# Performance work log

Hardware: AMD Instinct MI355X
Metric: run time of the kernel (lower is better)

## Reference

```python
import jax, jax.numpy as jnp
import numpy as np

N = 50000      # num_nodes
E = 400000     # num_edges
H = 64         # h_dim
R = 200        # num_rels
B = 8          # num_bases (block-diagonal decomposition)


def setup_inputs() -> dict:
    ks = jax.random.split(jax.random.key(0), 10)
    s = 1.0 / np.sqrt(H).astype(np.float32)
    return {
        "emb":     jax.random.normal(ks[0], (N, H), jnp.float32),
        "norm":    jax.random.uniform(ks[1], (E, 1), jnp.float32),
        "eps":     jax.random.normal(ks[2], (N, H), jnp.float32),
        "w1":      jax.random.normal(ks[3], (R, B * 8 * 8), jnp.float32) * s,
        "loop_w1": jax.random.normal(ks[4], (H, H), jnp.float32) * s,
        "b1":      jnp.zeros((H,), jnp.float32),
        "w2":      jax.random.normal(ks[5], (R, B * 8 * 16), jnp.float32) * s,
        "loop_w2": jax.random.normal(ks[6], (H, 2 * H), jnp.float32) * s,
        "b2":      jnp.zeros((2 * H,), jnp.float32),
        "h_ids":   jnp.arange(N, dtype=jnp.int32),
        "src":     jax.random.randint(ks[7], (E,), 0, N, jnp.int32),
        "dst":     jax.random.randint(ks[8], (E,), 0, N, jnp.int32),
        "rel":     jax.random.randint(ks[9], (E,), 0, R, jnp.int32),
    }


def bdd_conv(feat, src, dst, rel, norm, weight, loop_w, bias, out_feat):
    # RelGraphConv with 'bdd' regularizer: per-edge relation-indexed
    # block-diagonal weight gather, bmm message, norm scale, scatter-add,
    # then bias + self-loop.
    n_edges = src.shape[0]
    sub_in = feat.shape[1] // B
    sub_out = out_feat // B
    w = weight[rel].reshape(n_edges, B, sub_in, sub_out)   # gather per edge
    x = feat[src].reshape(n_edges, B, sub_in)
    msg = jnp.einsum('ebi,ebio->ebo', x, w).reshape(n_edges, out_feat) * norm
    agg = jax.ops.segment_sum(msg, dst, num_segments=feat.shape[0])
    return agg + bias + feat @ loop_w


def reference(emb, norm, eps, w1, loop_w1, b1, w2, loop_w2, b2,
              h_ids, src, dst, rel):
    feat = emb[h_ids]                                       # embedding lookup
    h1 = jax.nn.relu(bdd_conv(feat, src, dst, rel, norm, w1, loop_w1, b1, H))
    h2 = bdd_conv(h1, src, dst, rel, norm, w2, loop_w2, b2, 2 * H)
    m, raw_v = jnp.split(h2, 2, axis=-1)                    # gaussian_parameters
    v = jax.nn.softplus(raw_v) + 1e-8
    return m + jnp.sqrt(v) * eps                            # reparameterize
```

## Files before the change

kernel.cpp:

```cpp
#include <hip/hip_runtime.h>
#include <math.h>


typedef __attribute__((ext_vector_type(8))) short bf16x8;
typedef __attribute__((ext_vector_type(4))) float f32x4;
typedef __attribute__((ext_vector_type(2))) _Float16 h2;

__device__ __forceinline__ int bcasti(int v, int l) { return __builtin_amdgcn_readlane(v, l); }
__device__ __forceinline__ float bcastf(float v, int l) {
    return __int_as_float(__builtin_amdgcn_readlane(__float_as_int(v), l));
}
__device__ __forceinline__ unsigned short f2bf(float f) {
    unsigned u = __float_as_uint(f);
    return (unsigned short)((u + 0x7FFFu + ((u >> 16) & 1u)) >> 16);
}
__device__ __forceinline__ unsigned short f2h16(float f) {
    return __builtin_bit_cast(unsigned short, (_Float16)f);
}
__device__ __forceinline__ float bfs(unsigned short s) { return __uint_as_float((unsigned)s << 16); }
__device__ __forceinline__ h2 uh2(unsigned u) { return __builtin_bit_cast(h2, u); }


__global__ __launch_bounds__(256) void
blockhist(const int* __restrict__ dst, const int* __restrict__ rel,
          int* __restrict__ deg, int* __restrict__ bh, int R, int NB2, int e) {
    __shared__ int h[256];
    int t = threadIdx.x, b = blockIdx.x;
    h[t] = 0;
    __syncthreads();
    int base = b * 1024;
#pragma unroll
    for (int k = 0; k < 4; ++k) {
        int i = base + k * 256 + t;
        if (i < e) {
            atomicAdd(&deg[dst[i]], 1);
            atomicAdd(&h[rel[i]], 1);
        }
    }
    __syncthreads();
    if (t < R) bh[(size_t)t * NB2 + b] = h[t];
}

__global__ __launch_bounds__(256) void
rel_scan(int* __restrict__ bh, int* __restrict__ degr, int NB2) {
    __shared__ int sm[256];
    int r = blockIdx.x, t = threadIdx.x;
    int carry = 0;
    for (int s = 0; s < NB2; s += 256) {
        int idx = s + t;
        int v = (idx < NB2) ? bh[(size_t)r * NB2 + idx] : 0;
        sm[t] = v;
        __syncthreads();
        for (int d = 1; d < 256; d <<= 1) {
            int u = (t >= d) ? sm[t - d] : 0;
            __syncthreads();
            sm[t] += u;
            __syncthreads();
        }
        if (idx < NB2) bh[(size_t)r * NB2 + idx] = carry + sm[t] - v;
        int tot = sm[255];
        __syncthreads();
        carry += tot;
    }
    if (t == 0) degr[r] = carry;
}

__global__ void scan_part(const int* __restrict__ deg, int* __restrict__ bsum, int n) {
    __shared__ int sm[256];
    int t = threadIdx.x, g = blockIdx.x * 256 + t;
    sm[t] = (g < n) ? deg[g] : 0;
    __syncthreads();
    for (int d = 128; d > 0; d >>= 1) {
        if (t < d) sm[t] += sm[t + d];
        __syncthreads();
    }
    if (t == 0) bsum[blockIdx.x] = sm[0];
}

__global__ void scan_bsum(int* __restrict__ bsum, int* __restrict__ off, int nb, int n) {
    __shared__ int sm[256];
    int t = threadIdx.x;
    int v = (t < nb) ? bsum[t] : 0;
    sm[t] = v;
    __syncthreads();
    for (int d = 1; d < 256; d <<= 1) {
        int u = (t >= d) ? sm[t - d] : 0;
        __syncthreads();
        sm[t] += u;
        __syncthreads();
    }
    if (t < nb) bsum[t] = sm[t] - v;
    if (t == 255) off[n] = sm[255];
}

__global__ void scan_write(const int* __restrict__ deg, const int* __restrict__ bsum,
                           int* __restrict__ off, int n) {
    __shared__ int sm[256];
    int t = threadIdx.x, g = blockIdx.x * 256 + t;
    int v = (g < n) ? deg[g] : 0;
    sm[t] = v;
    __syncthreads();
    for (int d = 1; d < 256; d <<= 1) {
        int u = (t >= d) ? sm[t - d] : 0;
        __syncthreads();
        sm[t] += u;
        __syncthreads();
    }
    if (g < n) off[g] = bsum[blockIdx.x] + sm[t] - v;
}

__global__ void scan_rel(const int* __restrict__ degr, int* __restrict__ offr, int R) {
    __shared__ int sm[256];
    int t = threadIdx.x;
    int v = (t < R) ? degr[t] : 0;
    sm[t] = v;
    __syncthreads();
    for (int d = 1; d < 256; d <<= 1) {
        int u = (t >= d) ? sm[t - d] : 0;
        __syncthreads();
        sm[t] += u;
        __syncthreads();
    }
    if (t < R) offr[t] = sm[t] - v;
    if (t == 255) offr[R] = sm[255];
}

__global__ __launch_bounds__(256) void
scatter3(const int* __restrict__ src, const int* __restrict__ dst,
         const int* __restrict__ rel, const float* __restrict__ norm,
         const int* __restrict__ h_ids, const int* __restrict__ off,
         const int* __restrict__ offr, const int* __restrict__ bh,
         int* __restrict__ fil, int* __restrict__ pos,
         int* __restrict__ xidA, int* __restrict__ xidB,
         float* __restrict__ nrm, int NB2, int e) {
    __shared__ int h[256];
    int t = threadIdx.x, b = blockIdx.x;
    h[t] = 0;
    __syncthreads();
    int base = b * 1024;
#pragma unroll
    for (int k = 0; k < 4; ++k) {
        int i = base + k * 256 + t;
        if (i < e) {
            int r = rel[i], d = dst[i], s = src[i];
            int lr = atomicAdd(&h[r], 1);
            int p = offr[r] + bh[(size_t)r * NB2 + b] + lr;
            int q = off[d] + atomicAdd(&fil[d], 1);
            pos[q] = p;
            xidA[p] = h_ids[s];
            xidB[p] = s;
            nrm[p] = norm[i];
        }
    }
}


__global__ void cvt_new(const float* __restrict__ w1, const float* __restrict__ w2,
                        const float* __restrict__ emb, unsigned short* __restrict__ w1dT,
                        unsigned short* __restrict__ w2dT, unsigned short* __restrict__ embh,
                        int R, int ne) {
    int i = blockIdx.x * blockDim.x + threadIdx.x;
    int n1d = R * 4096, n2d = R * 8192;
    if (i < n1d) {
        int r = i >> 12, rem = i & 4095;
        int c = rem >> 6, k = rem & 63;
        int b = k >> 3;
        float v = (b == (c >> 3)) ? w1[(size_t)r * 512 + b * 64 + (k & 7) * 8 + (c & 7)] : 0.f;
        w1dT[i] = f2bf(v);
    } else if (i < n1d + n2d) {
        int ii = i - n1d;
        int r = ii >> 13, rem = ii & 8191;
        int c = rem >> 6, k = rem & 63;
        int b = k >> 3;
        float v = (b == (c >> 4)) ? w2[(size_t)r * 1024 + b * 128 + (k & 7) * 16 + (c & 15)] : 0.f;
        w2dT[ii] = f2bf(v);
    } else if (i < n1d + n2d + ne) {
        int ii = i - n1d - n2d;
        embh[ii] = f2bf(emb[ii]);
    }
}

__global__ void cvt_old(const float* __restrict__ w1, const float* __restrict__ w2,
                        const float* __restrict__ emb, unsigned short* __restrict__ w1h,
                        unsigned short* __restrict__ w2h, unsigned short* __restrict__ embh,
                        int n1, int n2, int ne) {
    int i = blockIdx.x * blockDim.x + threadIdx.x;
    if (i < n1) w1h[i] = f2h16(w1[i]);
    else if (i < n1 + n2) w2h[i - n1] = f2h16(w2[i - n1]);
    else if (i < n1 + n2 + ne) embh[i - n1 - n2] = f2bf(emb[i - n1 - n2]);
}


__global__ __launch_bounds__(256) void
gemm1_mfma(const unsigned short* __restrict__ embh, const int* __restrict__ h_ids,
           const float* __restrict__ lw1, const float* __restrict__ b1,
           unsigned short* __restrict__ h1bh, int n_nodes) {
    int w = threadIdx.x >> 6, l = threadIdx.x & 63;
    int lr = l & 15, lq = l >> 4;
    int rt = blockIdx.x;
    bf16x8 bfr[2];
    int coln = w * 16 + lr;
#pragma unroll
    for (int kb = 0; kb < 2; ++kb)
#pragma unroll
        for (int jj = 0; jj < 8; ++jj)
            bfr[kb][jj] = (short)f2bf(lw1[(kb * 32 + lq * 8 + jj) * 64 + coln]);
    int nrow = rt * 16 + lr;
    if (nrow >= n_nodes) nrow = n_nodes - 1;
    const unsigned short* arow = embh + (long)h_ids[nrow] * 64 + lq * 8;
    bf16x8 af0 = *(const bf16x8*)arow;
    bf16x8 af1 = *(const bf16x8*)(arow + 32);
    f32x4 acc = {0.f, 0.f, 0.f, 0.f};
    acc = __builtin_amdgcn_mfma_f32_16x16x32_bf16(af0, bfr[0], acc, 0, 0, 0);
    acc = __builtin_amdgcn_mfma_f32_16x16x32_bf16(af1, bfr[1], acc, 0, 0, 0);
    float bb = b1[coln];
#pragma unroll
    for (int r = 0; r < 4; ++r) {
        int row = rt * 16 + lq * 4 + r;
        if (row < n_nodes) h1bh[(long)row * 64 + coln] = f2bf(acc[r] + bb);
    }
}

__global__ __launch_bounds__(256) void
gemm2_mfma(const unsigned short* __restrict__ h1h, const float* __restrict__ lw2,
           const float* __restrict__ b2, unsigned short* __restrict__ h2bh, int n_nodes) {
    int w = threadIdx.x >> 6, l = threadIdx.x & 63;
    int lr = l & 15, lq = l >> 4;
    int rt = blockIdx.x;
    bf16x8 bfr[2][2];
    int col0 = (2 * w) * 16 + lr, col1 = (2 * w + 1) * 16 + lr;
#pragma unroll
    for (int kb = 0; kb < 2; ++kb)
#pragma unroll
        for (int jj = 0; jj < 8; ++jj) {
            int k = kb * 32 + lq * 8 + jj;
            bfr[0][kb][jj] = (short)f2bf(lw2[k * 128 + col0]);
            bfr[1][kb][jj] = (short)f2bf(lw2[k * 128 + col1]);
        }
    int nrow = rt * 16 + lr;
    if (nrow >= n_nodes) nrow = n_nodes - 1;
    bf16x8 af0 = *(const bf16x8*)(h1h + (long)nrow * 64 + lq * 8);
    bf16x8 af1 = *(const bf16x8*)(h1h + (long)nrow * 64 + 32 + lq * 8);
    f32x4 acc0 = {0.f, 0.f, 0.f, 0.f}, acc1 = {0.f, 0.f, 0.f, 0.f};
    acc0 = __builtin_amdgcn_mfma_f32_16x16x32_bf16(af0, bfr[0][0], acc0, 0, 0, 0);
    acc0 = __builtin_amdgcn_mfma_f32_16x16x32_bf16(af1, bfr[0][1], acc0, 0, 0, 0);
    acc1 = __builtin_amdgcn_mfma_f32_16x16x32_bf16(af0, bfr[1][0], acc1, 0, 0, 0);
    acc1 = __builtin_amdgcn_mfma_f32_16x16x32_bf16(af1, bfr[1][1], acc1, 0, 0, 0);
    float bb0 = b2[col0], bb1 = b2[col1];
#pragma unroll
    for (int r = 0; r < 4; ++r) {
        int row = rt * 16 + lq * 4 + r;
        if (row < n_nodes) {
            h2bh[(long)row * 128 + col0] = f2bf(acc0[r] + bb0);
            h2bh[(long)row * 128 + col1] = f2bf(acc1[r] + bb1);
        }
    }
}


__global__ __launch_bounds__(256) void
gemm_rel1(const unsigned short* __restrict__ embh, const unsigned short* __restrict__ w1dT,
          const int* __restrict__ xidA, const float* __restrict__ nrm,
          const int* __restrict__ offr, _Float16* __restrict__ msg1, int S) {
    int r = blockIdx.x / S, s = blockIdx.x % S;
    int w = threadIdx.x >> 6, l = threadIdx.x & 63;
    int lr = l & 15, lq = l >> 4;
    int e0r = offr[r], e1r = offr[r + 1];
    if (e0r >= e1r) return;
    bf16x8 bfr[4][2];
    const unsigned short* wb = w1dT + (size_t)r * 4096;
#pragma unroll
    for (int ct = 0; ct < 4; ++ct)
#pragma unroll
        for (int kb = 0; kb < 2; ++kb)
            bfr[ct][kb] = *(const bf16x8*)(wb + (ct * 16 + lr) * 64 + kb * 32 + lq * 8);
    for (int t = s * 4 + w;; t += S * 4) {
        int t16 = e0r + t * 16;
        if (t16 >= e1r) break;
        int erow = t16 + lr;
        int erc = erow < e1r ? erow : e1r - 1;
        const unsigned short* arow = embh + (size_t)xidA[erc] * 64 + lq * 8;
        bf16x8 af0 = *(const bf16x8*)arow;
        bf16x8 af1 = *(const bf16x8*)(arow + 32);
        f32x4 acc[4];
#pragma unroll
        for (int ct = 0; ct < 4; ++ct) {
            acc[ct] = (f32x4){0.f, 0.f, 0.f, 0.f};
            acc[ct] = __builtin_amdgcn_mfma_f32_16x16x32_bf16(af0, bfr[ct][0], acc[ct], 0, 0, 0);
            acc[ct] = __builtin_amdgcn_mfma_f32_16x16x32_bf16(af1, bfr[ct][1], acc[ct], 0, 0, 0);
        }
#pragma unroll
        for (int r4 = 0; r4 < 4; ++r4) {
            int orow = t16 + lq * 4 + r4;
            int orc = orow < e1r ? orow : e1r - 1;
            float nm = nrm[orc];
            if (orow < e1r) {
#pragma unroll
                for (int ct = 0; ct < 4; ++ct)
                    msg1[(size_t)orow * 64 + ct * 16 + lr] = (_Float16)(acc[ct][r4] * nm);
            }
        }
    }
}

__global__ __launch_bounds__(256) void
gemm_rel2(const unsigned short* __restrict__ h1h, const unsigned short* __restrict__ w2dT,
          const int* __restrict__ xidB, const float* __restrict__ nrm,
          const int* __restrict__ offr, _Float16* __restrict__ msg2, int S) {
    int r = blockIdx.x / S, s = blockIdx.x % S;
    int w = threadIdx.x >> 6, l = threadIdx.x & 63;
    int lr = l & 15, lq = l >> 4;
    int e0r = offr[r], e1r = offr[r + 1];
    if (e0r >= e1r) return;
    bf16x8 bfr[8][2];
    const unsigned short* wb = w2dT + (size_t)r * 8192;
#pragma unroll
    for (int ct = 0; ct < 8; ++ct)
#pragma unroll
        for (int kb = 0; kb < 2; ++kb)
            bfr[ct][kb] = *(const bf16x8*)(wb + (ct * 16 + lr) * 64 + kb * 32 + lq * 8);
    for (int t = s * 4 + w;; t += S * 4) {
        int t16 = e0r + t * 16;
        if (t16 >= e1r) break;
        int erow = t16 + lr;
        int erc = erow < e1r ? erow : e1r - 1;
        const unsigned short* arow = h1h + (size_t)xidB[erc] * 64 + lq * 8;
        bf16x8 af0 = *(const bf16x8*)arow;
        bf16x8 af1 = *(const bf16x8*)(arow + 32);
        f32x4 acc[8];
#pragma unroll
        for (int ct = 0; ct < 8; ++ct) {
            acc[ct] = (f32x4){0.f, 0.f, 0.f, 0.f};
            acc[ct] = __builtin_amdgcn_mfma_f32_16x16x32_bf16(af0, bfr[ct][0], acc[ct], 0, 0, 0);
            acc[ct] = __builtin_amdgcn_mfma_f32_16x16x32_bf16(af1, bfr[ct][1], acc[ct], 0, 0, 0);
        }
#pragma unroll
        for (int r4 = 0; r4 < 4; ++r4) {
            int orow = t16 + lq * 4 + r4;
            int orc = orow < e1r ? orow : e1r - 1;
            float nm = nrm[orc];
            if (orow < e1r) {
#pragma unroll
                for (int ct = 0; ct < 8; ++ct)
                    msg2[(size_t)orow * 128 + ct * 16 + lr] = (_Float16)(acc[ct][r4] * nm);
            }
        }
    }
}


__global__ __launch_bounds__(256) void
sum1(const _Float16* __restrict__ msg1, const int* __restrict__ pos,
     const unsigned short* __restrict__ h1bh, const int* __restrict__ off,
     unsigned short* __restrict__ h1h, int n_nodes) {
    int tid = threadIdx.x;
    int w = tid >> 6, j = tid & 63;
    int n = blockIdx.x * 4 + w;
    if (n >= n_nodes) return;
    float base = bfs(h1bh[(size_t)n * 64 + j]);
    int e0 = off[n], e1v = off[n + 1];
    float a0 = 0.f, a1 = 0.f, a2 = 0.f, a3 = 0.f;
    for (int win = e0; win < e1v; win += 64) {
        int wcnt = e1v - win; if (wcnt > 64) wcnt = 64;
        int pv = (j < wcnt) ? pos[win + j] : 0;
        int c = 0;
        for (; c + 4 <= wcnt; c += 4) {
            int p0 = bcasti(pv, c), p1 = bcasti(pv, c + 1);
            int p2 = bcasti(pv, c + 2), p3 = bcasti(pv, c + 3);
            a0 += (float)msg1[(size_t)p0 * 64 + j];
            a1 += (float)msg1[(size_t)p1 * 64 + j];
            a2 += (float)msg1[(size_t)p2 * 64 + j];
            a3 += (float)msg1[(size_t)p3 * 64 + j];
        }
        for (; c < wcnt; ++c)
            a0 += (float)msg1[(size_t)bcasti(pv, c) * 64 + j];
    }
    float s = a0 + a1 + a2 + a3 + base;
    h1h[(size_t)n * 64 + j] = f2bf(fmaxf(s, 0.f));
}

__global__ __launch_bounds__(256) void
sum2(const _Float16* __restrict__ msg2, const int* __restrict__ pos,
     const unsigned short* __restrict__ h2bh, const float* __restrict__ eps,
     const int* __restrict__ off, float* __restrict__ out, int n_nodes) {
    int tid = threadIdx.x;
    int w = tid >> 6, j = tid & 63;
    int n = blockIdx.x * 4 + w;
    if (n >= n_nodes) return;
    float basem = bfs(h2bh[(size_t)n * 128 + j]);
    float basev = bfs(h2bh[(size_t)n * 128 + 64 + j]);
    int e0 = off[n], e1v = off[n + 1];
    float m0 = 0.f, m1 = 0.f, v0 = 0.f, v1a = 0.f;
    for (int win = e0; win < e1v; win += 64) {
        int wcnt = e1v - win; if (wcnt > 64) wcnt = 64;
        int pv = (j < wcnt) ? pos[win + j] : 0;
        int c = 0;
        for (; c + 2 <= wcnt; c += 2) {
            int p0 = bcasti(pv, c), p1 = bcasti(pv, c + 1);
            m0 += (float)msg2[(size_t)p0 * 128 + j];
            v0 += (float)msg2[(size_t)p0 * 128 + 64 + j];
            m1 += (float)msg2[(size_t)p1 * 128 + j];
            v1a += (float)msg2[(size_t)p1 * 128 + 64 + j];
        }
        for (; c < wcnt; ++c) {
            int p0 = bcasti(pv, c);
            m0 += (float)msg2[(size_t)p0 * 128 + j];
            v0 += (float)msg2[(size_t)p0 * 128 + 64 + j];
        }
    }
    float vm = m0 + m1 + basem;
    float vv = v0 + v1a + basev;
    float sp = (vv > 20.f) ? vv : log1pf(expf(vv));
    out[(size_t)n * 64 + j] = fmaf(sqrtf(sp + 1e-8f), eps[(size_t)n * 64 + j], vm);
}


__global__ void hist2(const int* __restrict__ dst, const int* __restrict__ rel,
                      int* __restrict__ deg, int* __restrict__ degr, int e) {
    int i = blockIdx.x * blockDim.x + threadIdx.x;
    if (i < e) {
        atomicAdd(&deg[dst[i]], 1);
        atomicAdd(&degr[rel[i]], 1);
    }
}

__global__ void scatter_pack(const int* __restrict__ src, const int* __restrict__ dst,
                             const int* __restrict__ rel, const float* __restrict__ norm,
                             const int* __restrict__ h_ids, const int* __restrict__ off,
                             int* __restrict__ fil, unsigned* __restrict__ packA,
                             unsigned* __restrict__ packB, float* __restrict__ norm_s, int e) {
    int i = blockIdx.x * blockDim.x + threadIdx.x;
    if (i >= e) return;
    int d = dst[i];
    int p = off[d] + atomicAdd(&fil[d], 1);
    unsigned rhi = (unsigned)rel[i] << 16;
    int s = src[i];
    packA[p] = (unsigned)h_ids[s] | rhi;
    packB[p] = (unsigned)s | rhi;
    norm_s[p] = norm[i];
}

__device__ __forceinline__ float reduce8(float a0, float a1, float a2, float a3,
                                         float a4, float a5, float a6, float a7, int i) {
    int p1 = i & 1, p2 = (i >> 1) & 1, p3 = (i >> 2) & 1;
    float ka, sb, u0, u1, u2, u3, w0, w1;
    ka = p1 ? a1 : a0; sb = p1 ? a0 : a1; u0 = ka + __shfl_xor(sb, 1, 64);
    ka = p1 ? a3 : a2; sb = p1 ? a2 : a3; u1 = ka + __shfl_xor(sb, 1, 64);
    ka = p1 ? a5 : a4; sb = p1 ? a4 : a5; u2 = ka + __shfl_xor(sb, 1, 64);
    ka = p1 ? a7 : a6; sb = p1 ? a6 : a7; u3 = ka + __shfl_xor(sb, 1, 64);
    ka = p2 ? u1 : u0; sb = p2 ? u0 : u1; w0 = ka + __shfl_xor(sb, 2, 64);
    ka = p2 ? u3 : u2; sb = p2 ? u2 : u3; w1 = ka + __shfl_xor(sb, 2, 64);
    ka = p3 ? w1 : w0; sb = p3 ? w0 : w1;
    return ka + __shfl_xor(sb, 4, 64);
}

__global__ __launch_bounds__(256) void
edge1(const unsigned short* __restrict__ embh, const unsigned short* __restrict__ w1h,
      const unsigned short* __restrict__ h1bh, const int* __restrict__ off,
      const unsigned* __restrict__ packA, const float* __restrict__ norm_s,
      unsigned short* __restrict__ h1h, int n_nodes) {
    __shared__ unsigned short xstage[4][8][64];
    int tid = threadIdx.x;
    int w = tid >> 6, j = tid & 63, i = j & 7;
    int cl = j >> 3, il = j & 7;
    int n = blockIdx.x * 4 + w;
    if (n >= n_nodes) return;
    unsigned short* xsw = &xstage[w][0][0];
    float base = bfs(h1bh[(long)n * 64 + j]);
    h2 acc[4];
#pragma unroll
    for (int q = 0; q < 4; ++q) acc[q] = (h2){(_Float16)0.f, (_Float16)0.f};
    int e0 = off[n], e1v = off[n + 1];
    const long woff = (long)j * 8;
    for (int win = e0; win < e1v; win += 64) {
        int wcnt = e1v - win; if (wcnt > 64) wcnt = 64;
        unsigned u = (j < wcnt) ? packA[win + j] : 0u;
        float nmv = (j < wcnt) ? norm_s[win + j] : 0.f;
        for (int b8 = 0; b8 < wcnt; b8 += 8) {
            int cnt = wcnt - b8; if (cnt > 8) cnt = 8;
            int uc = __builtin_amdgcn_ds_bpermute((b8 + cl) << 2, (int)u);
            if (cl < cnt)
                *(bf16x8*)(xsw + (cl << 6) + (il << 3)) =
                    *(const bf16x8*)(embh + (long)((unsigned)uc & 0xFFFFu) * 64 + (il << 3));
            asm volatile("s_waitcnt lgkmcnt(0)" ::: "memory");
#pragma unroll
            for (int c = 0; c < 8; ++c)
                if (c < cnt) {
                    float nm = bcastf(nmv, b8 + c);
                    int rr = bcasti((int)u, b8 + c) >> 16;
                    uint4 wd = *(const uint4*)(w1h + (long)rr * 512 + woff);
                    _Float16 xh = (_Float16)(bfs(xsw[(c << 6) + j]) * nm);
                    h2 xh2 = {xh, xh};
                    acc[0] += xh2 * uh2(wd.x);
                    acc[1] += xh2 * uh2(wd.y);
                    acc[2] += xh2 * uh2(wd.z);
                    acc[3] += xh2 * uh2(wd.w);
                }
        }
    }
    float agg = reduce8((float)acc[0].x, (float)acc[0].y, (float)acc[1].x, (float)acc[1].y,
                        (float)acc[2].x, (float)acc[2].y, (float)acc[3].x, (float)acc[3].y, i);
    h1h[(long)n * 64 + j] = f2bf(fmaxf(base + agg, 0.f));
}

__global__ __launch_bounds__(256) void
edge2(const unsigned short* __restrict__ h1h, const unsigned short* __restrict__ w2h,
      const unsigned short* __restrict__ h2bh, const float* __restrict__ eps,
      const int* __restrict__ off, const unsigned* __restrict__ packB,
      const float* __restrict__ norm_s, float* __restrict__ out, int n_nodes) {
    __shared__ unsigned short xstage[4][8][64];
    int tid = threadIdx.x;
    int w = tid >> 6, j = tid & 63;
    int i = j & 7, b = j >> 3;
    int o1 = b * 16 + i, o2 = o1 + 8;
    int cl = j >> 3, il = j & 7;
    int n = blockIdx.x * 4 + w;
    if (n >= n_nodes) return;
    unsigned short* xsw = &xstage[w][0][0];
    float base1 = bfs(h2bh[(long)n * 128 + o1]);
    float base2 = bfs(h2bh[(long)n * 128 + o2]);
    h2 acc[8];
#pragma unroll
    for (int q = 0; q < 8; ++q) acc[q] = (h2){(_Float16)0.f, (_Float16)0.f};
    int e0 = off[n], e1v = off[n + 1];
    const long woff = (long)j * 16;
    for (int win = e0; win < e1v; win += 64) {
        int wcnt = e1v - win; if (wcnt > 64) wcnt = 64;
        unsigned u = (j < wcnt) ? packB[win + j] : 0u;
        float nmv = (j < wcnt) ? norm_s[win + j] : 0.f;
        for (int b8 = 0; b8 < wcnt; b8 += 8) {
            int cnt = wcnt - b8; if (cnt > 8) cnt = 8;
            int uc = __builtin_amdgcn_ds_bpermute((b8 + cl) << 2, (int)u);
            if (cl < cnt)
                *(bf16x8*)(xsw + (cl << 6) + (il << 3)) =
                    *(const bf16x8*)(h1h + (long)((unsigned)uc & 0xFFFFu) * 64 + (il << 3));
            asm volatile("s_waitcnt lgkmcnt(0)" ::: "memory");
#pragma unroll
            for (int c = 0; c < 8; ++c)
                if (c < cnt) {
                    float nm = bcastf(nmv, b8 + c);
                    int rr = bcasti((int)u, b8 + c) >> 16;
                    const uint4* p = (const uint4*)(w2h + (long)rr * 1024 + woff);
                    uint4 wa = p[0], wb = p[1];
                    _Float16 xh = (_Float16)(bfs(xsw[(c << 6) + j]) * nm);
                    h2 xh2 = {xh, xh};
                    acc[0] += xh2 * uh2(wa.x);
                    acc[1] += xh2 * uh2(wa.y);
                    acc[2] += xh2 * uh2(wa.z);
                    acc[3] += xh2 * uh2(wa.w);
                    acc[4] += xh2 * uh2(wb.x);
                    acc[5] += xh2 * uh2(wb.y);
                    acc[6] += xh2 * uh2(wb.z);
                    acc[7] += xh2 * uh2(wb.w);
                }
        }
    }
    float r1 = reduce8((float)acc[0].x, (float)acc[0].y, (float)acc[1].x, (float)acc[1].y,
                       (float)acc[2].x, (float)acc[2].y, (float)acc[3].x, (float)acc[3].y, i);
    float r2 = reduce8((float)acc[4].x, (float)acc[4].y, (float)acc[5].x, (float)acc[5].y,
                       (float)acc[6].x, (float)acc[6].y, (float)acc[7].x, (float)acc[7].y, i);
    float v1 = r1 + base1;
    float v2 = r2 + base2;
    float p1 = __shfl_xor(v1, 32, 64);
    float p2 = __shfl_xor(v2, 32, 64);
    if (j < 32) {
        long basep = (long)n * 64;
        float sp1 = (p1 > 20.f) ? p1 : log1pf(expf(p1));
        float sp2 = (p2 > 20.f) ? p2 : log1pf(expf(p2));
        out[basep + o1] = fmaf(sqrtf(sp1 + 1e-8f), eps[basep + o1], v1);
        out[basep + o2] = fmaf(sqrtf(sp2 + 1e-8f), eps[basep + o2], v2);
    }
}


extern "C" void kernel_launch(void* const* d_in, const int* in_sizes, int n_in,
                              void* d_out, int out_size, void* d_ws, size_t ws_size,
                              hipStream_t stream) {
    const float* emb   = (const float*)d_in[0];
    const float* norm  = (const float*)d_in[1];
    const float* eps   = (const float*)d_in[2];
    const float* w1    = (const float*)d_in[3];
    const float* lw1   = (const float*)d_in[4];
    const float* b1    = (const float*)d_in[5];
    const float* w2    = (const float*)d_in[6];
    const float* lw2   = (const float*)d_in[7];
    const float* b2    = (const float*)d_in[8];
    const int*   h_ids = (const int*)d_in[9];
    const int*   src   = (const int*)d_in[10];
    const int*   dst   = (const int*)d_in[11];
    const int*   rel   = (const int*)d_in[12];
    float* out = (float*)d_out;

    int n_nodes = in_sizes[0] / 64;
    int n_edges = in_sizes[10];
    int nw1 = in_sizes[3];
    int nw2 = in_sizes[6];
    int ne  = in_sizes[0];
    int R   = nw1 / 512;

    int blk = 256;
    int nb = (n_nodes + 255) / 256;
    int nt = (n_nodes + 15) / 16;
    int ng = (n_nodes + 3) / 4;
    int NB2 = (n_edges + 1023) / 1024;

    size_t need = (size_t)ne * 2
                + (size_t)n_nodes * 64 * 2 * 2
                + (size_t)n_nodes * 128 * 2
                + (size_t)R * 4096 * 2
                + (size_t)R * 8192 * 2
                + (size_t)n_edges * 4 * 4
                + (size_t)n_edges * 128 * 2
                + (size_t)(2 * n_nodes + R) * 4
                + (size_t)R * NB2 * 4
                + (size_t)(n_nodes + 1) * 4
                + (size_t)(R + 1) * 4
                + (size_t)nb * 4;

    if (ws_size >= need && R <= 256) {
        char* p = (char*)d_ws;
        unsigned short* embh = (unsigned short*)p;  p += (size_t)ne * 2;
        unsigned short* h1bh = (unsigned short*)p;  p += (size_t)n_nodes * 64 * 2;
        unsigned short* h1h  = (unsigned short*)p;  p += (size_t)n_nodes * 64 * 2;
        unsigned short* h2bh = (unsigned short*)p;  p += (size_t)n_nodes * 128 * 2;
        unsigned short* w1dT = (unsigned short*)p;  p += (size_t)R * 4096 * 2;
        unsigned short* w2dT = (unsigned short*)p;  p += (size_t)R * 8192 * 2;
        int*   xidA = (int*)p;                      p += (size_t)n_edges * 4;
        int*   xidB = (int*)p;                      p += (size_t)n_edges * 4;
        float* nrm  = (float*)p;                    p += (size_t)n_edges * 4;
        int*   pos  = (int*)p;                      p += (size_t)n_edges * 4;
        _Float16* msg = (_Float16*)p;               p += (size_t)n_edges * 128 * 2;
        int* deg  = (int*)p;                        p += (size_t)n_nodes * 4;
        int* fil  = (int*)p;                        p += (size_t)n_nodes * 4;
        int* degr = (int*)p;                        p += (size_t)R * 4;
        int* bh   = (int*)p;                        p += (size_t)R * NB2 * 4;
        int* off  = (int*)p;                        p += (size_t)(n_nodes + 1) * 4;
        int* offr = (int*)p;                        p += (size_t)(R + 1) * 4;
        int* bsum = (int*)p;

        const int S = 8;
        int ncv = R * 4096 + R * 8192 + ne;
        hipMemsetAsync(deg, 0, (size_t)(2 * n_nodes) * 4, stream);
        cvt_new<<<(ncv + blk - 1) / blk, blk, 0, stream>>>(w1, w2, emb, w1dT, w2dT, embh, R, ne);
        blockhist<<<NB2, blk, 0, stream>>>(dst, rel, deg, bh, R, NB2, n_edges);
        scan_part<<<nb, 256, 0, stream>>>(deg, bsum, n_nodes);
        scan_bsum<<<1, 256, 0, stream>>>(bsum, off, nb, n_nodes);
        scan_write<<<nb, 256, 0, stream>>>(deg, bsum, off, n_nodes);
        rel_scan<<<R, 256, 0, stream>>>(bh, degr, NB2);
        scan_rel<<<1, 256, 0, stream>>>(degr, offr, R);
        scatter3<<<NB2, blk, 0, stream>>>(src, dst, rel, norm, h_ids, off, offr, bh,
                                          fil, pos, xidA, xidB, nrm, NB2, n_edges);
        gemm1_mfma<<<nt, blk, 0, stream>>>(embh, h_ids, lw1, b1, h1bh, n_nodes);
        gemm_rel1<<<R * S, blk, 0, stream>>>(embh, w1dT, xidA, nrm, offr, msg, S);
        sum1<<<ng, blk, 0, stream>>>(msg, pos, h1bh, off, h1h, n_nodes);
        gemm2_mfma<<<nt, blk, 0, stream>>>(h1h, lw2, b2, h2bh, n_nodes);
        gemm_rel2<<<R * S, blk, 0, stream>>>(h1h, w2dT, xidB, nrm, offr, msg, S);
        sum2<<<ng, blk, 0, stream>>>(msg, pos, h2bh, eps, off, out, n_nodes);
    } else {
        char* p = (char*)d_ws;
        unsigned short* h1bh = (unsigned short*)p;  p += (size_t)n_nodes * 64 * 2;
        unsigned short* h1h  = (unsigned short*)p;  p += (size_t)n_nodes * 64 * 2;
        unsigned short* h2bh = (unsigned short*)p;  p += (size_t)n_nodes * 128 * 2;
        unsigned short* embh = (unsigned short*)p;  p += (size_t)ne * 2;
        unsigned short* w1h  = (unsigned short*)p;  p += (size_t)nw1 * 2;
        unsigned short* w2h  = (unsigned short*)p;  p += (size_t)nw2 * 2;
        unsigned* pkA = (unsigned*)p;               p += (size_t)n_edges * 4;
        unsigned* pkB = (unsigned*)p;               p += (size_t)n_edges * 4;
        float* norm_s = (float*)p;                  p += (size_t)n_edges * 4;
        int* deg  = (int*)p;                        p += (size_t)n_nodes * 4;
        int* fil  = (int*)p;                        p += (size_t)n_nodes * 4;
        int* degr = (int*)p;                        p += (size_t)R * 4;
        int* filr = (int*)p;                        p += (size_t)R * 4;
        int* off  = (int*)p;                        p += (size_t)(n_nodes + 1) * 4;
        int* bsum = (int*)p;

        hipMemsetAsync(deg, 0, (size_t)(2 * n_nodes + 2 * R) * 4, stream);
        cvt_old<<<(nw1 + nw2 + ne + blk - 1) / blk, blk, 0, stream>>>(w1, w2, emb, w1h, w2h, embh, nw1, nw2, ne);
        hist2<<<(n_edges + blk - 1) / blk, blk, 0, stream>>>(dst, rel, deg, degr, n_edges);
        scan_part<<<nb, 256, 0, stream>>>(deg, bsum, n_nodes);
        scan_bsum<<<1, 256, 0, stream>>>(bsum, off, nb, n_nodes);
        scan_write<<<nb, 256, 0, stream>>>(deg, bsum, off, n_nodes);
        scatter_pack<<<(n_edges + blk - 1) / blk, blk, 0, stream>>>(
            src, dst, rel, norm, h_ids, off, fil, pkA, pkB, norm_s, n_edges);
        gemm1_mfma<<<nt, blk, 0, stream>>>(embh, h_ids, lw1, b1, h1bh, n_nodes);
        edge1<<<ng, blk, 0, stream>>>(embh, w1h, h1bh, off, pkA, norm_s, h1h, n_nodes);
        gemm2_mfma<<<nt, blk, 0, stream>>>(h1h, lw2, b2, h2bh, n_nodes);
        edge2<<<ng, blk, 0, stream>>>(h1h, w2h, h2bh, eps, off, pkB, norm_s, out, n_nodes);
    }
}
```

Baseline: 308.0 us.

## Write messages in destination order and pack per-edge metadata into int4

The relation GEMM kernels now scatter each message row straight to its destination-sorted slot q. That lets the sum kernels read messages contiguously instead of indirectly through a pos array. Per-edge source ids, norm and the destination slot are packed into one int4 record, replacing four separate arrays. Histogram and scatter blocks now handle 256 edges instead of 1024, and the GEMM split factor S is raised from 8 to 16. The cost moves from gathered reads in the reductions to scattered writes in the GEMM kernels.

```diff
diff --git a/kernel.cpp b/kernel.cpp
--- a/kernel.cpp
+++ b/kernel.cpp
@@ -28,14 +28,10 @@
     int t = threadIdx.x, b = blockIdx.x;
     h[t] = 0;
     __syncthreads();
-    int base = b * 1024;
-#pragma unroll
-    for (int k = 0; k < 4; ++k) {
-        int i = base + k * 256 + t;
-        if (i < e) {
-            atomicAdd(&deg[dst[i]], 1);
-            atomicAdd(&h[rel[i]], 1);
-        }
+    int i = b * 256 + t;
+    if (i < e) {
+        atomicAdd(&deg[dst[i]], 1);
+        atomicAdd(&h[rel[i]], 1);
     }
     __syncthreads();
     if (t < R) bh[(size_t)t * NB2 + b] = h[t];
@@ -130,27 +126,23 @@
          const int* __restrict__ rel, const float* __restrict__ norm,
          const int* __restrict__ h_ids, const int* __restrict__ off,
          const int* __restrict__ offr, const int* __restrict__ bh,
-         int* __restrict__ fil, int* __restrict__ pos,
-         int* __restrict__ xidA, int* __restrict__ xidB,
-         float* __restrict__ nrm, int NB2, int e) {
+         int* __restrict__ fil, int4* __restrict__ epk, int NB2, int e) {
     __shared__ int h[256];
     int t = threadIdx.x, b = blockIdx.x;
     h[t] = 0;
     __syncthreads();
-    int base = b * 1024;
-#pragma unroll
-    for (int k = 0; k < 4; ++k) {
-        int i = base + k * 256 + t;
-        if (i < e) {
-            int r = rel[i], d = dst[i], s = src[i];
-            int lr = atomicAdd(&h[r], 1);
-            int p = offr[r] + bh[(size_t)r * NB2 + b] + lr;
-            int q = off[d] + atomicAdd(&fil[d], 1);
-            pos[q] = p;
-            xidA[p] = h_ids[s];
-            xidB[p] = s;
-            nrm[p] = norm[i];
-        }
+    int i = b * 256 + t;
+    if (i < e) {
+        int r = rel[i], d = dst[i], s = src[i];
+        int lrk = atomicAdd(&h[r], 1);
+        int p = offr[r] + bh[(size_t)r * NB2 + b] + lrk;
+        int q = off[d] + atomicAdd(&fil[d], 1);
+        int4 v;
+        v.x = h_ids[s];
+        v.y = s;
+        v.z = __float_as_int(norm[i]);
+        v.w = q;
+        epk[p] = v;
     }
 }
 
@@ -260,8 +252,8 @@
 
 __global__ __launch_bounds__(256) void
 gemm_rel1(const unsigned short* __restrict__ embh, const unsigned short* __restrict__ w1dT,
-          const int* __restrict__ xidA, const float* __restrict__ nrm,
-          const int* __restrict__ offr, _Float16* __restrict__ msg1, int S) {
+          const int4* __restrict__ epk, const int* __restrict__ offr,
+          _Float16* __restrict__ msg1, int S) {
     int r = blockIdx.x / S, s = blockIdx.x % S;
     int w = threadIdx.x >> 6, l = threadIdx.x & 63;
     int lr = l & 15, lq = l >> 4;
@@ -279,7 +271,8 @@
         if (t16 >= e1r) break;
         int erow = t16 + lr;
         int erc = erow < e1r ? erow : e1r - 1;
-        const unsigned short* arow = embh + (size_t)xidA[erc] * 64 + lq * 8;
+        int xa = epk[erc].x;
+        const unsigned short* arow = embh + (size_t)xa * 64 + lq * 8;
         bf16x8 af0 = *(const bf16x8*)arow;
         bf16x8 af1 = *(const bf16x8*)(arow + 32);
         f32x4 acc[4];
@@ -293,11 +286,13 @@
         for (int r4 = 0; r4 < 4; ++r4) {
             int orow = t16 + lq * 4 + r4;
             int orc = orow < e1r ? orow : e1r - 1;
-            float nm = nrm[orc];
+            int2 nq = *(const int2*)(&epk[orc].z);
+            float nm = __int_as_float(nq.x);
+            size_t q = (size_t)nq.y;
             if (orow < e1r) {
 #pragma unroll
                 for (int ct = 0; ct < 4; ++ct)
-                    msg1[(size_t)orow * 64 + ct * 16 + lr] = (_Float16)(acc[ct][r4] * nm);
+                    msg1[q * 64 + ct * 16 + lr] = (_Float16)(acc[ct][r4] * nm);
             }
         }
     }
@@ -305,8 +300,8 @@
 
 __global__ __launch_bounds__(256) void
 gemm_rel2(const unsigned short* __restrict__ h1h, const unsigned short* __restrict__ w2dT,
-          const int* __restrict__ xidB, const float* __restrict__ nrm,
-          const int* __restrict__ offr, _Float16* __restrict__ msg2, int S) {
+          const int4* __restrict__ epk, const int* __restrict__ offr,
+          _Float16* __restrict__ msg2, int S) {
     int r = blockIdx.x / S, s = blockIdx.x % S;
     int w = threadIdx.x >> 6, l = threadIdx.x & 63;
     int lr = l & 15, lq = l >> 4;
@@ -324,7 +319,8 @@
         if (t16 >= e1r) break;
         int erow = t16 + lr;
         int erc = erow < e1r ? erow : e1r - 1;
-        const unsigned short* arow = h1h + (size_t)xidB[erc] * 64 + lq * 8;
+        int xb = epk[erc].y;
+        const unsigned short* arow = h1h + (size_t)xb * 64 + lq * 8;
         bf16x8 af0 = *(const bf16x8*)arow;
         bf16x8 af1 = *(const bf16x8*)(arow + 32);
         f32x4 acc[8];
@@ -338,11 +334,13 @@
         for (int r4 = 0; r4 < 4; ++r4) {
             int orow = t16 + lq * 4 + r4;
             int orc = orow < e1r ? orow : e1r - 1;
-            float nm = nrm[orc];
+            int2 nq = *(const int2*)(&epk[orc].z);
+            float nm = __int_as_float(nq.x);
+            size_t q = (size_t)nq.y;
             if (orow < e1r) {
 #pragma unroll
                 for (int ct = 0; ct < 8; ++ct)
-                    msg2[(size_t)orow * 128 + ct * 16 + lr] = (_Float16)(acc[ct][r4] * nm);
+                    msg2[q * 128 + ct * 16 + lr] = (_Float16)(acc[ct][r4] * nm);
             }
         }
     }
@@ -350,9 +348,8 @@
 
 
 __global__ __launch_bounds__(256) void
-sum1(const _Float16* __restrict__ msg1, const int* __restrict__ pos,
-     const unsigned short* __restrict__ h1bh, const int* __restrict__ off,
-     unsigned short* __restrict__ h1h, int n_nodes) {
+sum1(const _Float16* __restrict__ msg1, const unsigned short* __restrict__ h1bh,
+     const int* __restrict__ off, unsigned short* __restrict__ h1h, int n_nodes) {
     int tid = threadIdx.x;
     int w = tid >> 6, j = tid & 63;
     int n = blockIdx.x * 4 + w;
@@ -360,29 +357,21 @@
     float base = bfs(h1bh[(size_t)n * 64 + j]);
     int e0 = off[n], e1v = off[n + 1];
     float a0 = 0.f, a1 = 0.f, a2 = 0.f, a3 = 0.f;
-    for (int win = e0; win < e1v; win += 64) {
-        int wcnt = e1v - win; if (wcnt > 64) wcnt = 64;
-        int pv = (j < wcnt) ? pos[win + j] : 0;
-        int c = 0;
-        for (; c + 4 <= wcnt; c += 4) {
-            int p0 = bcasti(pv, c), p1 = bcasti(pv, c + 1);
-            int p2 = bcasti(pv, c + 2), p3 = bcasti(pv, c + 3);
-            a0 += (float)msg1[(size_t)p0 * 64 + j];
-            a1 += (float)msg1[(size_t)p1 * 64 + j];
-            a2 += (float)msg1[(size_t)p2 * 64 + j];
-            a3 += (float)msg1[(size_t)p3 * 64 + j];
-        }
-        for (; c < wcnt; ++c)
-            a0 += (float)msg1[(size_t)bcasti(pv, c) * 64 + j];
-    }
-    float s = a0 + a1 + a2 + a3 + base;
-    h1h[(size_t)n * 64 + j] = f2bf(fmaxf(s, 0.f));
-}
-
-__global__ __launch_bounds__(256) void
-sum2(const _Float16* __restrict__ msg2, const int* __restrict__ pos,
-     const unsigned short* __restrict__ h2bh, const float* __restrict__ eps,
-     const int* __restrict__ off, float* __restrict__ out, int n_nodes) {
+    int r = e0;
+    for (; r + 4 <= e1v; r += 4) {
+        a0 += (float)msg1[(size_t)(r + 0) * 64 + j];
+        a1 += (float)msg1[(size_t)(r + 1) * 64 + j];
+        a2 += (float)msg1[(size_t)(r + 2) * 64 + j];
+        a3 += (float)msg1[(size_t)(r + 3) * 64 + j];
+    }
+    for (; r < e1v; ++r) a0 += (float)msg1[(size_t)r * 64 + j];
+    h1h[(size_t)n * 64 + j] = f2bf(fmaxf(a0 + a1 + a2 + a3 + base, 0.f));
+}
+
+__global__ __launch_bounds__(256) void
+sum2(const _Float16* __restrict__ msg2, const unsigned short* __restrict__ h2bh,
+     const float* __restrict__ eps, const int* __restrict__ off,
+     float* __restrict__ out, int n_nodes) {
     int tid = threadIdx.x;
     int w = tid >> 6, j = tid & 63;
     int n = blockIdx.x * 4 + w;
@@ -391,22 +380,16 @@
     float basev = bfs(h2bh[(size_t)n * 128 + 64 + j]);
     int e0 = off[n], e1v = off[n + 1];
     float m0 = 0.f, m1 = 0.f, v0 = 0.f, v1a = 0.f;
-    for (int win = e0; win < e1v; win += 64) {
-        int wcnt = e1v - win; if (wcnt > 64) wcnt = 64;
-        int pv = (j < wcnt) ? pos[win + j] : 0;
-        int c = 0;
-        for (; c + 2 <= wcnt; c += 2) {
-            int p0 = bcasti(pv, c), p1 = bcasti(pv, c + 1);
-            m0 += (float)msg2[(size_t)p0 * 128 + j];
-            v0 += (float)msg2[(size_t)p0 * 128 + 64 + j];
-            m1 += (float)msg2[(size_t)p1 * 128 + j];
-            v1a += (float)msg2[(size_t)p1 * 128 + 64 + j];
-        }
-        for (; c < wcnt; ++c) {
-            int p0 = bcasti(pv, c);
-            m0 += (float)msg2[(size_t)p0 * 128 + j];
-            v0 += (float)msg2[(size_t)p0 * 128 + 64 + j];
-        }
+    int r = e0;
+    for (; r + 2 <= e1v; r += 2) {
+        m0  += (float)msg2[(size_t)(r + 0) * 128 + j];
+        v0  += (float)msg2[(size_t)(r + 0) * 128 + 64 + j];
+        m1  += (float)msg2[(size_t)(r + 1) * 128 + j];
+        v1a += (float)msg2[(size_t)(r + 1) * 128 + 64 + j];
+    }
+    for (; r < e1v; ++r) {
+        m0 += (float)msg2[(size_t)r * 128 + j];
+        v0 += (float)msg2[(size_t)r * 128 + 64 + j];
     }
     float vm = m0 + m1 + basem;
     float vv = v0 + v1a + basev;
@@ -602,14 +585,14 @@
     int nb = (n_nodes + 255) / 256;
     int nt = (n_nodes + 15) / 16;
     int ng = (n_nodes + 3) / 4;
-    int NB2 = (n_edges + 1023) / 1024;
+    int NB2 = (n_edges + 255) / 256;
 
     size_t need = (size_t)ne * 2
                 + (size_t)n_nodes * 64 * 2 * 2
                 + (size_t)n_nodes * 128 * 2
                 + (size_t)R * 4096 * 2
                 + (size_t)R * 8192 * 2
-                + (size_t)n_edges * 4 * 4
+                + (size_t)n_edges * 16
                 + (size_t)n_edges * 128 * 2
                 + (size_t)(2 * n_nodes + R) * 4
                 + (size_t)R * NB2 * 4
@@ -625,10 +608,7 @@
         unsigned short* h2bh = (unsigned short*)p;  p += (size_t)n_nodes * 128 * 2;
         unsigned short* w1dT = (unsigned short*)p;  p += (size_t)R * 4096 * 2;
         unsigned short* w2dT = (unsigned short*)p;  p += (size_t)R * 8192 * 2;
-        int*   xidA = (int*)p;                      p += (size_t)n_edges * 4;
-        int*   xidB = (int*)p;                      p += (size_t)n_edges * 4;
-        float* nrm  = (float*)p;                    p += (size_t)n_edges * 4;
-        int*   pos  = (int*)p;                      p += (size_t)n_edges * 4;
+        int4*  epk = (int4*)p;                      p += (size_t)n_edges * 16;
         _Float16* msg = (_Float16*)p;               p += (size_t)n_edges * 128 * 2;
         int* deg  = (int*)p;                        p += (size_t)n_nodes * 4;
         int* fil  = (int*)p;                        p += (size_t)n_nodes * 4;
@@ -638,7 +618,7 @@
         int* offr = (int*)p;                        p += (size_t)(R + 1) * 4;
         int* bsum = (int*)p;
 
-        const int S = 8;
+        const int S = 16;
         int ncv = R * 4096 + R * 8192 + ne;
         hipMemsetAsync(deg, 0, (size_t)(2 * n_nodes) * 4, stream);
         cvt_new<<<(ncv + blk - 1) / blk, blk, 0, stream>>>(w1, w2, emb, w1dT, w2dT, embh, R, ne);
@@ -649,13 +629,13 @@
         rel_scan<<<R, 256, 0, stream>>>(bh, degr, NB2);
         scan_rel<<<1, 256, 0, stream>>>(degr, offr, R);
         scatter3<<<NB2, blk, 0, stream>>>(src, dst, rel, norm, h_ids, off, offr, bh,
-                                          fil, pos, xidA, xidB, nrm, NB2, n_edges);
+                                          fil, epk, NB2, n_edges);
         gemm1_mfma<<<nt, blk, 0, stream>>>(embh, h_ids, lw1, b1, h1bh, n_nodes);
-        gemm_rel1<<<R * S, blk, 0, stream>>>(embh, w1dT, xidA, nrm, offr, msg, S);
-        sum1<<<ng, blk, 0, stream>>>(msg, pos, h1bh, off, h1h, n_nodes);
+        gemm_rel1<<<R * S, blk, 0, stream>>>(embh, w1dT, epk, offr, msg, S);
+        sum1<<<ng, blk, 0, stream>>>(msg, h1bh, off, h1h, n_nodes);
         gemm2_mfma<<<nt, blk, 0, stream>>>(h1h, lw2, b2, h2bh, n_nodes);
-        gemm_rel2<<<R * S, blk, 0, stream>>>(h1h, w2dT, xidB, nrm, offr, msg, S);
-        sum2<<<ng, blk, 0, stream>>>(msg, pos, h2bh, eps, off, out, n_nodes);
+        gemm_rel2<<<R * S, blk, 0, stream>>>(h1h, w2dT, epk, offr, msg, S);
+        sum2<<<ng, blk, 0, stream>>>(msg, h2bh, eps, off, out, n_nodes);
     } else {
         char* p = (char*)d_ws;
         unsigned short* h1bh = (unsigned short*)p;  p += (size_t)n_nodes * 64 * 2;
```

After: 318.6 us. 3.4% more time.
